# Kernel optimization log

Measured on AMD Instinct MI355X. Metric: run time of the kernel, lower is better.

The kernel has to match this reference:

```python
import jax, jax.numpy as jnp
import numpy as np

N, E, F_IN, H, G, A, OUT = 50000, 800000, 128, 256, 64, 8, 1


def _lin(k, fi, fo):
    s = 1.0 / np.sqrt(fi)
    kw, kb = jax.random.split(k)
    W = jax.random.uniform(kw, (fi, fo), jnp.float32, -s, s)
    b = jax.random.uniform(kb, (fo,), jnp.float32, -s, s)
    return W, b


def setup_inputs() -> dict:
    key = jax.random.key(0)
    ks = jax.random.split(key, 12)
    x = jax.random.normal(ks[0], (N, F_IN), jnp.float32)
    edge_index = jax.random.randint(ks[1], (2, E), 0, N, dtype=jnp.int64)
    batch = jnp.sort(jax.random.randint(ks[2], (N,), 0, G, dtype=jnp.int64))
    graph_attr = jax.random.normal(ks[3], (G, A), jnp.float32)
    W1, b1 = _lin(ks[4], F_IN, H)
    W2, b2 = _lin(ks[5], H, H)
    W3, b3 = _lin(ks[6], H, H)
    fcW1, fcb1 = _lin(ks[7], H + A, H)
    fcW2, fcb2 = _lin(ks[8], H, OUT)
    ones = jnp.ones((H,), jnp.float32)
    zeros = jnp.zeros((H,), jnp.float32)
    return dict(x=x, graph_attr=graph_attr, edge_index=edge_index, batch=batch,
                W1=W1, b1=b1, W2=W2, b2=b2, W3=W3, b3=b3,
                g1=ones, be1=zeros, g2=ones, be2=zeros, g3=ones, be3=zeros,
                fcW1=fcW1, fcb1=fcb1, fcW2=fcW2, fcb2=fcb2)


def gcn_conv(x, W, b, src, dst, n):
    # PyG GCNConv: add self-loops, symmetric normalization, xW then scatter-add
    xw = x @ W  # [N, H]
    loop = jnp.arange(n)
    src2 = jnp.concatenate([src, loop])
    dst2 = jnp.concatenate([dst, loop])
    deg = jnp.zeros((n,), xw.dtype).at[dst2].add(1.0)
    dinv = jnp.where(deg > 0, jax.lax.rsqrt(deg), 0.0)
    norm = dinv[src2] * dinv[dst2]  # [E+N]
    out = jnp.zeros((n, xw.shape[1]), xw.dtype).at[dst2].add(xw[src2] * norm[:, None])
    return out + b


def layer_norm(x, g, b, eps=1e-5):
    m = x.mean(-1, keepdims=True)
    v = ((x - m) ** 2).mean(-1, keepdims=True)
    return (x - m) * jax.lax.rsqrt(v + eps) * g + b


def reference(x, graph_attr, edge_index, batch,
              W1, b1, W2, b2, W3, b3,
              g1, be1, g2, be2, g3, be3,
              fcW1, fcb1, fcW2, fcb2):
    src, dst = edge_index[0], edge_index[1]
    h = jax.nn.relu(layer_norm(gcn_conv(x, W1, b1, src, dst, N), g1, be1))
    h = jax.nn.relu(layer_norm(gcn_conv(h, W2, b2, src, dst, N), g2, be2))
    h = jax.nn.relu(layer_norm(gcn_conv(h, W3, b3, src, dst, N), g3, be3))
    # global mean pool over graph ids
    sums = jax.ops.segment_sum(h, batch, num_segments=G)
    cnts = jax.ops.segment_sum(jnp.ones((N,), h.dtype), batch, num_segments=G)
    pooled = sums / jnp.maximum(cnts, 1.0)[:, None]  # [G, H]
    z = jnp.concatenate([pooled, graph_attr.reshape(-1, A)], axis=1)
    z = jax.nn.relu(z @ fcW1 + fcb1)
    return z @ fcW2 + fcb2  # [G, OUT]
```

## Files before the change

### kernel.cpp

```cpp
#include <hip/hip_runtime.h>
#include <hip/hip_bf16.h>

#define N_NODES 50000
#define N_EDGES 800000
#define F_IN    128
#define H_DIM   256
#define G_NUM   64
#define A_DIM   8

typedef __attribute__((ext_vector_type(8))) short short8v;
typedef __attribute__((ext_vector_type(4))) float float4v;
typedef __attribute__((ext_vector_type(2))) float float2v;

__device__ __forceinline__ float b2f(unsigned short u) {
    return __uint_as_float(((unsigned int)u) << 16);
}
__device__ __forceinline__ unsigned short f2b(float v) {
    return __hip_bfloat16_raw(__float2bfloat16(v)).x;
}
__device__ __forceinline__ unsigned char f2fp8(float v) {
    return (unsigned char)(__builtin_amdgcn_cvt_pk_fp8_f32(v, v, 0, false) & 0xff);
}
__device__ __forceinline__ unsigned int pack2(float a, float b) {
    return (unsigned int)f2b(a) | ((unsigned int)f2b(b) << 16);
}
__device__ __forceinline__ void accadd16(float2v* a, uint4 v) {
    a[0] += __builtin_amdgcn_cvt_pk_f32_fp8((int)v.x, false);
    a[1] += __builtin_amdgcn_cvt_pk_f32_fp8((int)v.x, true);
    a[2] += __builtin_amdgcn_cvt_pk_f32_fp8((int)v.y, false);
    a[3] += __builtin_amdgcn_cvt_pk_f32_fp8((int)v.y, true);
    a[4] += __builtin_amdgcn_cvt_pk_f32_fp8((int)v.z, false);
    a[5] += __builtin_amdgcn_cvt_pk_f32_fp8((int)v.z, true);
    a[6] += __builtin_amdgcn_cvt_pk_f32_fp8((int)v.w, false);
    a[7] += __builtin_amdgcn_cvt_pk_f32_fp8((int)v.w, true);
}
__device__ __forceinline__ void accadd8(float2v* a, uint2 v) {
    a[0] += __builtin_amdgcn_cvt_pk_f32_fp8((int)v.x, false);
    a[1] += __builtin_amdgcn_cvt_pk_f32_fp8((int)v.x, true);
    a[2] += __builtin_amdgcn_cvt_pk_f32_fp8((int)v.y, false);
    a[3] += __builtin_amdgcn_cvt_pk_f32_fp8((int)v.y, true);
}


__global__ void init_kernel(const int* __restrict__ dst, int* __restrict__ indeg,
                            const float* __restrict__ W1, unsigned short* __restrict__ Wt1,
                            const float* __restrict__ W2, unsigned short* __restrict__ Wt2,
                            const float* __restrict__ W3, unsigned short* __restrict__ Wt3) {
    const int EB = (N_EDGES + 255) / 256;
    const int n_w1 = F_IN * H_DIM;
    const int n_w2 = H_DIM * H_DIM;
    int b = blockIdx.x, t = threadIdx.x;
    if (b < EB) {
        int i = b * 256 + t;
        if (i < N_EDGES) atomicAdd(&indeg[dst[i]], 1);
        return;
    }
    int i = (b - EB) * 256 + t;
    if (i < n_w1) {
        int k = i / H_DIM, n = i % H_DIM;
        Wt1[(size_t)n * F_IN + k] = f2b(W1[i]);
    } else if (i < n_w1 + n_w2) {
        int j = i - n_w1;
        int k = j / H_DIM, n = j % H_DIM;
        Wt2[(size_t)n * H_DIM + k] = f2b(W2[j]);
    } else if (i < n_w1 + 2 * n_w2) {
        int j = i - n_w1 - n_w2;
        int k = j / H_DIM, n = j % H_DIM;
        Wt3[(size_t)n * H_DIM + k] = f2b(W3[j]);
    }
}


__global__ __launch_bounds__(256) void scan1_kernel(const int* __restrict__ in,
                                                    int* __restrict__ out,
                                                    int* __restrict__ bsum,
                                                    float* __restrict__ dinv, int n) {
    __shared__ int tile[256];
    int b = blockIdx.x, t = threadIdx.x, i = b * 256 + t;
    int v = (i < n) ? in[i] : 0;
    if (i < n) dinv[i] = rsqrtf((float)v + 1.0f);
    tile[t] = v;
    __syncthreads();
    #pragma unroll
    for (int o = 1; o < 256; o <<= 1) {
        int add = (t >= o) ? tile[t - o] : 0;
        __syncthreads();
        tile[t] += add;
        __syncthreads();
    }
    if (i < n) out[i] = tile[t] - v;
    if (t == 255) bsum[b] = tile[255];
}

__global__ __launch_bounds__(256) void scan2_kernel(int* __restrict__ bsum, int nb,
                                                    const int* __restrict__ batch,
                                                    int* __restrict__ gstart,
                                                    float* __restrict__ pooled) {
    __shared__ int tile[256];
    int t = threadIdx.x;
    int v = (t < nb) ? bsum[t] : 0;
    tile[t] = v;
    __syncthreads();
    #pragma unroll
    for (int o = 1; o < 256; o <<= 1) {
        int add = (t >= o) ? tile[t - o] : 0;
        __syncthreads();
        tile[t] += add;
        __syncthreads();
    }
    if (t < nb) bsum[t] = tile[t] - v;
    if (t <= G_NUM) {
        int lo = 0, hi = N_NODES;
        while (lo < hi) {
            int mid = (lo + hi) >> 1;
            if (batch[mid] < t) lo = mid + 1; else hi = mid;
        }
        gstart[t] = lo;
    }
    for (int i = t; i < G_NUM * H_DIM; i += 256) pooled[i] = 0.f;
}

__global__ __launch_bounds__(256) void scan3_kernel(int* __restrict__ out,
                                                    const int* __restrict__ bsum,
                                                    int* __restrict__ pos, int n) {
    int i = blockIdx.x * blockDim.x + threadIdx.x;
    if (i < n) {
        int r = out[i] + bsum[i >> 8];
        out[i] = r;
        pos[i] = r;
    }
    if (i == 0) out[n] = N_EDGES;
}


__global__ void place2_kernel(const int* __restrict__ src, const int* __restrict__ dst,
                              int* __restrict__ pos, unsigned short* __restrict__ csr_src,
                              const float4* __restrict__ x, unsigned int* __restrict__ xb8,
                              const float* __restrict__ dinv) {
    const int PB = (N_EDGES + 255) / 256;
    int b = blockIdx.x, t = threadIdx.x;
    if (b < PB) {
        int i = b * 256 + t;
        if (i < N_EDGES) {
            int s = src[i], dn = dst[i];
            int slot = atomicAdd(&pos[dn], 1);
            csr_src[slot] = (unsigned short)s;
        }
        return;
    }
    int i = (b - PB) * 256 + t;
    if (i < N_NODES * (F_IN / 4)) {
        float4 vv = x[i];
        float dv = dinv[i >> 5];
        unsigned int pk = (unsigned int)__builtin_amdgcn_cvt_pk_fp8_f32(vv.x * dv, vv.y * dv, 0, false);
        pk = (unsigned int)__builtin_amdgcn_cvt_pk_fp8_f32(vv.z * dv, vv.w * dv, (int)pk, true);
        xb8[i] = pk;
    }
}


#define SK 40

__global__ __launch_bounds__(512) void gemm_f8(const unsigned short* __restrict__ A,
                                               const unsigned short* __restrict__ Bt,
                                               unsigned char* __restrict__ C8,
                                               const float* __restrict__ dinv,
                                               int M, int K) {
    __shared__ unsigned short As[128][SK];
    __shared__ unsigned short Bs[256][SK];
    int t = threadIdx.x;
    int wave = t >> 6, lane = t & 63;
    int wm0 = (wave & 1) * 64, wn0 = (wave >> 1) * 64;
    int bm = blockIdx.x * 128;
    int l15 = lane & 15, lq = lane >> 4;
    float4v acc[4][4];
    #pragma unroll
    for (int i = 0; i < 4; i++)
        #pragma unroll
        for (int j = 0; j < 4; j++)
            acc[i][j] = (float4v){0.f, 0.f, 0.f, 0.f};

    for (int k0 = 0; k0 < K; k0 += 32) {
        {
            int row = t >> 2, koff = (t & 3) * 8;
            uint4 va = make_uint4(0u, 0u, 0u, 0u);
            if (bm + row < M)
                va = *(const uint4*)(A + (size_t)(bm + row) * K + k0 + koff);
            *(uint4*)&As[row][koff] = va;
        }
        #pragma unroll
        for (int h = 0; h < 2; h++) {
            int c = t + h * 512;
            int row = c >> 2, koff = (c & 3) * 8;
            uint4 vb = *(const uint4*)(Bt + (size_t)row * K + k0 + koff);
            *(uint4*)&Bs[row][koff] = vb;
        }
        __syncthreads();
        short8v af[4], bf[4];
        #pragma unroll
        for (int i = 0; i < 4; i++) {
            af[i] = *(const short8v*)&As[wm0 + i * 16 + l15][lq * 8];
            bf[i] = *(const short8v*)&Bs[wn0 + i * 16 + l15][lq * 8];
        }
        #pragma unroll
        for (int i = 0; i < 4; i++)
            #pragma unroll
            for (int j = 0; j < 4; j++)
                acc[i][j] = __builtin_amdgcn_mfma_f32_16x16x32_bf16(af[i], bf[j], acc[i][j], 0, 0, 0);
        __syncthreads();
    }
    #pragma unroll
    for (int i = 0; i < 4; i++) {
        #pragma unroll
        for (int r = 0; r < 4; r++) {
            int row = bm + wm0 + i * 16 + lq * 4 + r;
            if (row < M) {
                float dv = dinv[row];
                #pragma unroll
                for (int j = 0; j < 4; j++) {
                    int col = wn0 + j * 16 + l15;
                    C8[(size_t)row * H_DIM + col] = f2fp8(dv * acc[i][j][r]);
                }
            }
        }
    }
}


__global__ __launch_bounds__(512) void gemm_ln(const unsigned short* __restrict__ A,
                                               const unsigned short* __restrict__ Bt,
                                               unsigned short* __restrict__ C,
                                               const float* __restrict__ bias,
                                               const float* __restrict__ gamma,
                                               const float* __restrict__ beta,
                                               int M, int K) {
    __shared__ unsigned short As[128][SK];
    __shared__ unsigned short Bs[256][SK];
    __shared__ float red_s[4][128];
    __shared__ float red_ss[4][128];
    int t = threadIdx.x;
    int wave = t >> 6, lane = t & 63;
    int wm0 = (wave & 1) * 64, wn0 = (wave >> 1) * 64;
    int wn_idx = wave >> 1;
    int bm = blockIdx.x * 128;
    int l15 = lane & 15, lq = lane >> 4;
    float4v acc[4][4];
    #pragma unroll
    for (int i = 0; i < 4; i++)
        #pragma unroll
        for (int j = 0; j < 4; j++)
            acc[i][j] = (float4v){0.f, 0.f, 0.f, 0.f};

    for (int k0 = 0; k0 < K; k0 += 32) {
        {
            int row = t >> 2, koff = (t & 3) * 8;
            uint4 va = make_uint4(0u, 0u, 0u, 0u);
            if (bm + row < M)
                va = *(const uint4*)(A + (size_t)(bm + row) * K + k0 + koff);
            *(uint4*)&As[row][koff] = va;
        }
        #pragma unroll
        for (int h = 0; h < 2; h++) {
            int c = t + h * 512;
            int row = c >> 2, koff = (c & 3) * 8;
            uint4 vb = *(const uint4*)(Bt + (size_t)row * K + k0 + koff);
            *(uint4*)&Bs[row][koff] = vb;
        }
        __syncthreads();
        short8v af[4], bf[4];
        #pragma unroll
        for (int i = 0; i < 4; i++) {
            af[i] = *(const short8v*)&As[wm0 + i * 16 + l15][lq * 8];
            bf[i] = *(const short8v*)&Bs[wn0 + i * 16 + l15][lq * 8];
        }
        #pragma unroll
        for (int i = 0; i < 4; i++)
            #pragma unroll
            for (int j = 0; j < 4; j++)
                acc[i][j] = __builtin_amdgcn_mfma_f32_16x16x32_bf16(af[i], bf[j], acc[i][j], 0, 0, 0);
        __syncthreads();
    }

    float bcol[4], gcol[4], becol[4];
    #pragma unroll
    for (int j = 0; j < 4; j++) {
        int col = wn0 + j * 16 + l15;
        bcol[j] = bias[col]; gcol[j] = gamma[col]; becol[j] = beta[col];
    }
    #pragma unroll
    for (int i = 0; i < 4; i++) {
        #pragma unroll
        for (int r = 0; r < 4; r++) {
            float s = 0.f, ss = 0.f;
            #pragma unroll
            for (int j = 0; j < 4; j++) {
                float v = acc[i][j][r] + bcol[j];
                s += v; ss += v * v;
            }
            #pragma unroll
            for (int o = 1; o <= 8; o <<= 1) {
                s  += __shfl_xor(s, o, 64);
                ss += __shfl_xor(ss, o, 64);
            }
            if (l15 == 0) {
                int row = wm0 + i * 16 + lq * 4 + r;
                red_s[wn_idx][row] = s;
                red_ss[wn_idx][row] = ss;
            }
        }
    }
    __syncthreads();
    #pragma unroll
    for (int i = 0; i < 4; i++) {
        #pragma unroll
        for (int r = 0; r < 4; r++) {
            int lrow = wm0 + i * 16 + lq * 4 + r;
            int row = bm + lrow;
            if (row < M) {
                float S  = red_s[0][lrow] + red_s[1][lrow] + red_s[2][lrow] + red_s[3][lrow];
                float SS = red_ss[0][lrow] + red_ss[1][lrow] + red_ss[2][lrow] + red_ss[3][lrow];
                float mn = S * (1.f / H_DIM);
                float var = SS * (1.f / H_DIM) - mn * mn;
                float rstd = rsqrtf(var + 1e-5f);
                #pragma unroll
                for (int j = 0; j < 4; j++) {
                    int col = wn0 + j * 16 + l15;
                    float v = acc[i][j][r] + bcol[j];
                    float o = fmaxf((v - mn) * rstd * gcol[j] + becol[j], 0.f);
                    C[(size_t)row * H_DIM + col] = f2b(o);
                }
            }
        }
    }
}


template<int F, bool DO_LN>
__global__ __launch_bounds__(256) void gather_ns(const unsigned char* __restrict__ xw,
                                                 unsigned short* __restrict__ out,
                                                 const int* __restrict__ rowptr,
                                                 const unsigned short* __restrict__ csr_src,
                                                 const float* __restrict__ dinv,
                                                 const float* __restrict__ bias,
                                                 const float* __restrict__ gamma,
                                                 const float* __restrict__ beta) {
    constexpr int BPL = F / 16;
    constexpr int NF2 = BPL / 2;
    int lane = threadIdx.x & 63;
    int wave = threadIdx.x >> 6;
    int p = lane & 15;
    int gbase = lane & 48;
    int node = blockIdx.x * 16 + wave * 4 + (lane >> 4);
    int beg = rowptr[node];
    int deg = rowptr[node + 1] - beg;
    const unsigned char* xp = xw + (size_t)p * BPL;

    float2v acc2[NF2];
    #pragma unroll
    for (int k = 0; k < NF2; k++) acc2[k] = (float2v){0.f, 0.f};

    if constexpr (F == 256) {
        uint4 v = *(const uint4*)(xp + (size_t)node * F);
        accadd16(acc2, v);
    } else {
        uint2 v = *(const uint2*)(xp + (size_t)node * F);
        accadd8(acc2, v);
    }

    for (int b0 = 0; b0 < deg; b0 += 16) {
        int m = deg - b0; if (m > 16) m = 16;
        int sv = (p < m) ? (int)csr_src[beg + b0 + p] : 0;
        int j = 0;
        for (; j + 4 <= m; j += 4) {
            int s0 = __shfl(sv, gbase | j, 64);
            int s1 = __shfl(sv, gbase | (j + 1), 64);
            int s2 = __shfl(sv, gbase | (j + 2), 64);
            int s3 = __shfl(sv, gbase | (j + 3), 64);
            if constexpr (F == 256) {
                uint4 v0 = *(const uint4*)(xp + (size_t)s0 * F);
                uint4 v1 = *(const uint4*)(xp + (size_t)s1 * F);
                uint4 v2 = *(const uint4*)(xp + (size_t)s2 * F);
                uint4 v3 = *(const uint4*)(xp + (size_t)s3 * F);
                accadd16(acc2, v0); accadd16(acc2, v1);
                accadd16(acc2, v2); accadd16(acc2, v3);
            } else {
                uint2 v0 = *(const uint2*)(xp + (size_t)s0 * F);
                uint2 v1 = *(const uint2*)(xp + (size_t)s1 * F);
                uint2 v2 = *(const uint2*)(xp + (size_t)s2 * F);
                uint2 v3 = *(const uint2*)(xp + (size_t)s3 * F);
                accadd8(acc2, v0); accadd8(acc2, v1);
                accadd8(acc2, v2); accadd8(acc2, v3);
            }
        }
        for (; j < m; ++j) {
            int s0 = __shfl(sv, gbase | j, 64);
            if constexpr (F == 256) {
                uint4 v0 = *(const uint4*)(xp + (size_t)s0 * F);
                accadd16(acc2, v0);
            } else {
                uint2 v0 = *(const uint2*)(xp + (size_t)s0 * F);
                accadd8(acc2, v0);
            }
        }
    }

    float d = dinv[node];
    float v[BPL];
    #pragma unroll
    for (int k = 0; k < NF2; k++) { v[2 * k] = d * acc2[k].x; v[2 * k + 1] = d * acc2[k].y; }

    if constexpr (DO_LN) {
        #pragma unroll
        for (int q = 0; q < BPL / 4; q++) {
            float4 bi = ((const float4*)bias)[p * (BPL / 4) + q];
            v[q * 4 + 0] += bi.x; v[q * 4 + 1] += bi.y;
            v[q * 4 + 2] += bi.z; v[q * 4 + 3] += bi.w;
        }
        float s = 0.f, ss = 0.f;
        #pragma unroll
        for (int k = 0; k < BPL; k++) { s += v[k]; ss += v[k] * v[k]; }
        #pragma unroll
        for (int o = 1; o < 16; o <<= 1) {
            s  += __shfl_xor(s, o, 64);
            ss += __shfl_xor(ss, o, 64);
        }
        float mn = s * (1.f / F);
        float var = ss * (1.f / F) - mn * mn;
        float rstd = rsqrtf(var + 1e-5f);
        #pragma unroll
        for (int q = 0; q < BPL / 4; q++) {
            float4 ga = ((const float4*)gamma)[p * (BPL / 4) + q];
            float4 be = ((const float4*)beta)[p * (BPL / 4) + q];
            v[q * 4 + 0] = fmaxf((v[q * 4 + 0] - mn) * rstd * ga.x + be.x, 0.f);
            v[q * 4 + 1] = fmaxf((v[q * 4 + 1] - mn) * rstd * ga.y + be.y, 0.f);
            v[q * 4 + 2] = fmaxf((v[q * 4 + 2] - mn) * rstd * ga.z + be.z, 0.f);
            v[q * 4 + 3] = fmaxf((v[q * 4 + 3] - mn) * rstd * ga.w + be.w, 0.f);
        }
    }

    unsigned short* op = out + (size_t)node * F + p * BPL;
    uint4 o0;
    o0.x = pack2(v[0], v[1]); o0.y = pack2(v[2], v[3]);
    o0.z = pack2(v[4], v[5]); o0.w = pack2(v[6], v[7]);
    *(uint4*)op = o0;
    if constexpr (F == 256) {
        uint4 o1;
        o1.x = pack2(v[8],  v[9]);  o1.y = pack2(v[10], v[11]);
        o1.z = pack2(v[12], v[13]); o1.w = pack2(v[14], v[15]);
        *(uint4*)(op + 8) = o1;
    }
}


__global__ __launch_bounds__(128) void pool_kernel(const unsigned int* __restrict__ h32,
                                                   const int* __restrict__ batch,
                                                   float* __restrict__ pooled, int n) {
    int t = threadIdx.x;
    int start = blockIdx.x * 64;
    int end = min(start + 64, n);
    if (start >= n) return;
    int cur = batch[start];
    float a0 = 0.f, a1 = 0.f;
    for (int i = start; i < end; ++i) {
        int g = batch[i];
        if (g != cur) {
            atomicAdd(&pooled[(size_t)cur * H_DIM + 2 * t], a0);
            atomicAdd(&pooled[(size_t)cur * H_DIM + 2 * t + 1], a1);
            a0 = a1 = 0.f;
            cur = g;
        }
        unsigned int u = h32[(size_t)i * (H_DIM / 2) + t];
        a0 += b2f((unsigned short)(u & 0xffffu));
        a1 += b2f((unsigned short)(u >> 16));
    }
    atomicAdd(&pooled[(size_t)cur * H_DIM + 2 * t], a0);
    atomicAdd(&pooled[(size_t)cur * H_DIM + 2 * t + 1], a1);
}


__global__ __launch_bounds__(256) void fc_kernel(const float* __restrict__ pooled,
                                                 const int* __restrict__ gstart,
                                                 const float* __restrict__ gattr,
                                                 const float* __restrict__ fcW1,
                                                 const float* __restrict__ fcb1,
                                                 const float* __restrict__ fcW2,
                                                 const float* __restrict__ fcb2,
                                                 float* __restrict__ out) {
    __shared__ float zc[H_DIM + A_DIM];
    __shared__ float z1[H_DIM];
    int g = blockIdx.x, t = threadIdx.x;
    int c_i = gstart[g + 1] - gstart[g];
    float c = (float)(c_i > 1 ? c_i : 1);
    zc[t] = pooled[(size_t)g * H_DIM + t] / c;
    if (t < A_DIM) zc[H_DIM + t] = gattr[g * A_DIM + t];
    __syncthreads();
    float s = fcb1[t];
    for (int k = 0; k < H_DIM + A_DIM; k++)
        s += zc[k] * fcW1[(size_t)k * H_DIM + t];
    z1[t] = fmaxf(s, 0.f) * fcW2[t];
    __syncthreads();
    for (int off = 128; off; off >>= 1) {
        if (t < off) z1[t] += z1[t + off];
        __syncthreads();
    }
    if (t == 0) out[g] = z1[0] + fcb2[0];
}


extern "C" void kernel_launch(void* const* d_in, const int* in_sizes, int n_in,
                              void* d_out, int out_size, void* d_ws, size_t ws_size,
                              hipStream_t stream) {
    const float* x     = (const float*)d_in[0];
    const float* gattr = (const float*)d_in[1];
    const int*   ei    = (const int*)d_in[2];
    const int*   batch = (const int*)d_in[3];
    const float* W1 = (const float*)d_in[4];  const float* b1 = (const float*)d_in[5];
    const float* W2 = (const float*)d_in[6];  const float* b2 = (const float*)d_in[7];
    const float* W3 = (const float*)d_in[8];  const float* b3 = (const float*)d_in[9];
    const float* g1 = (const float*)d_in[10]; const float* be1 = (const float*)d_in[11];
    const float* g2 = (const float*)d_in[12]; const float* be2 = (const float*)d_in[13];
    const float* g3 = (const float*)d_in[14]; const float* be3 = (const float*)d_in[15];
    const float* fcW1 = (const float*)d_in[16]; const float* fcb1 = (const float*)d_in[17];
    const float* fcW2 = (const float*)d_in[18]; const float* fcb2 = (const float*)d_in[19];
    float* out = (float*)d_out;

    char* w = (char*)d_ws;
    unsigned char*  Pb8 = (unsigned char*)w;  w += (size_t)N_NODES * H_DIM;
    unsigned short* Hb  = (unsigned short*)w; w += (size_t)N_NODES * H_DIM * 2;
    unsigned char*  Xb8 = (unsigned char*)w;  w += (size_t)N_NODES * F_IN;
    unsigned short* AXb = (unsigned short*)w; w += (size_t)N_NODES * F_IN * 2;
    unsigned short* Wt1 = (unsigned short*)w; w += (size_t)H_DIM * F_IN * 2;
    unsigned short* Wt2 = (unsigned short*)w; w += (size_t)H_DIM * H_DIM * 2;
    unsigned short* Wt3 = (unsigned short*)w; w += (size_t)H_DIM * H_DIM * 2;
    float* dinv   = (float*)w; w += (size_t)N_NODES * 4;
    float* pooled = (float*)w; w += (size_t)G_NUM * H_DIM * 4;
    int* indeg    = (int*)w;   w += (size_t)N_NODES * 4;
    int* rowptr   = (int*)w;   w += (size_t)(N_NODES + 1) * 4;
    int* pos      = (int*)w;   w += (size_t)N_NODES * 4;
    unsigned short* csr_src = (unsigned short*)w; w += (size_t)N_EDGES * 2;
    int* gstart   = (int*)w;   w += (size_t)(G_NUM + 1) * 4;
    int* bsum     = (int*)w;   w += (size_t)256 * 4;

    const int* srcp = ei;
    const int* dstp = ei + N_EDGES;
    const int n_sblk = (N_NODES + 255) / 256;

    hipMemsetAsync(indeg, 0, (size_t)N_NODES * sizeof(int), stream);
    {
        const int EB = (N_EDGES + 255) / 256;
        int conv_tot = F_IN * H_DIM + 2 * H_DIM * H_DIM;
        int CB = (conv_tot + 255) / 256;
        init_kernel<<<EB + CB, 256, 0, stream>>>(dstp, indeg, W1, Wt1, W2, Wt2, W3, Wt3);
    }
    scan1_kernel<<<n_sblk, 256, 0, stream>>>(indeg, rowptr, bsum, dinv, N_NODES);
    scan2_kernel<<<1, 256, 0, stream>>>(bsum, n_sblk, batch, gstart, pooled);
    scan3_kernel<<<n_sblk, 256, 0, stream>>>(rowptr, bsum, pos, N_NODES);
    {
        const int PB = (N_EDGES + 255) / 256;
        const int CBX = (N_NODES * (F_IN / 4) + 255) / 256;
        place2_kernel<<<PB + CBX, 256, 0, stream>>>(srcp, dstp, pos, csr_src,
                                                    (const float4*)x, (unsigned int*)Xb8, dinv);
    }

    int gemm_blocks = (N_NODES + 127) / 128;
    int gather_blocks = N_NODES / 16;

    gather_ns<F_IN, false><<<gather_blocks, 256, 0, stream>>>(Xb8, AXb, rowptr, csr_src, dinv,
                                                              nullptr, nullptr, nullptr);
    gemm_ln<<<gemm_blocks, 512, 0, stream>>>(AXb, Wt1, Hb, b1, g1, be1, N_NODES, F_IN);

    gemm_f8<<<gemm_blocks, 512, 0, stream>>>(Hb, Wt2, Pb8, dinv, N_NODES, H_DIM);
    gather_ns<H_DIM, true><<<gather_blocks, 256, 0, stream>>>(Pb8, Hb, rowptr, csr_src, dinv,
                                                              b2, g2, be2);
    gemm_f8<<<gemm_blocks, 512, 0, stream>>>(Hb, Wt3, Pb8, dinv, N_NODES, H_DIM);
    gather_ns<H_DIM, true><<<gather_blocks, 256, 0, stream>>>(Pb8, Hb, rowptr, csr_src, dinv,
                                                              b3, g3, be3);

    pool_kernel<<<(N_NODES + 63) / 64, 128, 0, stream>>>((const unsigned int*)Hb, batch, pooled, N_NODES);
    fc_kernel<<<G_NUM, 256, 0, stream>>>(pooled, gstart, gattr, fcW1, fcb1, fcW2, fcb2, out);
}
```

Baseline: 381.3 us.

## Reorder layer 1 to GEMM-then-gather and fuse CSR placement into GEMM launch

Layer 1 now does the X·W1 GEMM first, writing dinv-scaled fp8 output, and then runs the 256-wide gather with the fused LayerNorm, the same order as layers 2 and 3. This replaces the old aggregate-then-GEMM path and removes the separate gemm_ln kernel. The in-degree atomic now records each edge's local slot, so CSR placement needs no second atomic pass. That placement runs as extra blocks inside the layer-1 GEMM launch, which removes the place2 kernel and the pos array. The cost is that the layer-1 gather moves 256 fp8 bytes per edge instead of 128, and x is now converted to bf16 in init_kernel.

```diff
diff --git a/kernel.cpp b/kernel.cpp
--- a/kernel.cpp
+++ b/kernel.cpp
@@ -34,39 +34,46 @@
     a[6] += __builtin_amdgcn_cvt_pk_f32_fp8((int)v.w, false);
     a[7] += __builtin_amdgcn_cvt_pk_f32_fp8((int)v.w, true);
 }
-__device__ __forceinline__ void accadd8(float2v* a, uint2 v) {
-    a[0] += __builtin_amdgcn_cvt_pk_f32_fp8((int)v.x, false);
-    a[1] += __builtin_amdgcn_cvt_pk_f32_fp8((int)v.x, true);
-    a[2] += __builtin_amdgcn_cvt_pk_f32_fp8((int)v.y, false);
-    a[3] += __builtin_amdgcn_cvt_pk_f32_fp8((int)v.y, true);
-}
 
 
 __global__ void init_kernel(const int* __restrict__ dst, int* __restrict__ indeg,
+                            unsigned short* __restrict__ eloc,
+                            const float4* __restrict__ x, uint2* __restrict__ xb,
                             const float* __restrict__ W1, unsigned short* __restrict__ Wt1,
                             const float* __restrict__ W2, unsigned short* __restrict__ Wt2,
                             const float* __restrict__ W3, unsigned short* __restrict__ Wt3) {
     const int EB = (N_EDGES + 255) / 256;
+    const int n_x4 = N_NODES * F_IN / 4;
     const int n_w1 = F_IN * H_DIM;
     const int n_w2 = H_DIM * H_DIM;
     int b = blockIdx.x, t = threadIdx.x;
     if (b < EB) {
         int i = b * 256 + t;
-        if (i < N_EDGES) atomicAdd(&indeg[dst[i]], 1);
+        if (i < N_EDGES)
+            eloc[i] = (unsigned short)atomicAdd(&indeg[dst[i]], 1);
         return;
     }
     int i = (b - EB) * 256 + t;
-    if (i < n_w1) {
-        int k = i / H_DIM, n = i % H_DIM;
-        Wt1[(size_t)n * F_IN + k] = f2b(W1[i]);
-    } else if (i < n_w1 + n_w2) {
-        int j = i - n_w1;
-        int k = j / H_DIM, n = j % H_DIM;
-        Wt2[(size_t)n * H_DIM + k] = f2b(W2[j]);
-    } else if (i < n_w1 + 2 * n_w2) {
-        int j = i - n_w1 - n_w2;
-        int k = j / H_DIM, n = j % H_DIM;
-        Wt3[(size_t)n * H_DIM + k] = f2b(W3[j]);
+    if (i < n_x4) {
+        float4 v = x[i];
+        uint2 o;
+        o.x = pack2(v.x, v.y);
+        o.y = pack2(v.z, v.w);
+        xb[i] = o;
+    } else {
+        int j = i - n_x4;
+        if (j < n_w1) {
+            int k = j / H_DIM, n = j % H_DIM;
+            Wt1[(size_t)n * F_IN + k] = f2b(W1[j]);
+        } else if (j < n_w1 + n_w2) {
+            int j2 = j - n_w1;
+            int k = j2 / H_DIM, n = j2 % H_DIM;
+            Wt2[(size_t)n * H_DIM + k] = f2b(W2[j2]);
+        } else if (j < n_w1 + 2 * n_w2) {
+            int j3 = j - n_w1 - n_w2;
+            int k = j3 / H_DIM, n = j3 % H_DIM;
+            Wt3[(size_t)n * H_DIM + k] = f2b(W3[j3]);
+        }
     }
 }
 
@@ -121,57 +128,25 @@
 }
 
 __global__ __launch_bounds__(256) void scan3_kernel(int* __restrict__ out,
-                                                    const int* __restrict__ bsum,
-                                                    int* __restrict__ pos, int n) {
+                                                    const int* __restrict__ bsum, int n) {
     int i = blockIdx.x * blockDim.x + threadIdx.x;
-    if (i < n) {
-        int r = out[i] + bsum[i >> 8];
-        out[i] = r;
-        pos[i] = r;
-    }
+    if (i < n) out[i] = out[i] + bsum[i >> 8];
     if (i == 0) out[n] = N_EDGES;
 }
 
 
-__global__ void place2_kernel(const int* __restrict__ src, const int* __restrict__ dst,
-                              int* __restrict__ pos, unsigned short* __restrict__ csr_src,
-                              const float4* __restrict__ x, unsigned int* __restrict__ xb8,
-                              const float* __restrict__ dinv) {
-    const int PB = (N_EDGES + 255) / 256;
-    int b = blockIdx.x, t = threadIdx.x;
-    if (b < PB) {
-        int i = b * 256 + t;
-        if (i < N_EDGES) {
-            int s = src[i], dn = dst[i];
-            int slot = atomicAdd(&pos[dn], 1);
-            csr_src[slot] = (unsigned short)s;
-        }
-        return;
-    }
-    int i = (b - PB) * 256 + t;
-    if (i < N_NODES * (F_IN / 4)) {
-        float4 vv = x[i];
-        float dv = dinv[i >> 5];
-        unsigned int pk = (unsigned int)__builtin_amdgcn_cvt_pk_fp8_f32(vv.x * dv, vv.y * dv, 0, false);
-        pk = (unsigned int)__builtin_amdgcn_cvt_pk_fp8_f32(vv.z * dv, vv.w * dv, (int)pk, true);
-        xb8[i] = pk;
-    }
-}
-
-
 #define SK 40
 
-__global__ __launch_bounds__(512) void gemm_f8(const unsigned short* __restrict__ A,
-                                               const unsigned short* __restrict__ Bt,
-                                               unsigned char* __restrict__ C8,
-                                               const float* __restrict__ dinv,
-                                               int M, int K) {
+__device__ __forceinline__ void gemm_body_f8(const unsigned short* __restrict__ A,
+                                             const unsigned short* __restrict__ Bt,
+                                             unsigned char* __restrict__ C8,
+                                             const float* __restrict__ dinv,
+                                             int M, int K, int bm) {
     __shared__ unsigned short As[128][SK];
     __shared__ unsigned short Bs[256][SK];
     int t = threadIdx.x;
     int wave = t >> 6, lane = t & 63;
     int wm0 = (wave & 1) * 64, wn0 = (wave >> 1) * 64;
-    int bm = blockIdx.x * 128;
     int l15 = lane & 15, lq = lane >> 4;
     float4v acc[4][4];
     #pragma unroll
@@ -226,111 +201,34 @@
     }
 }
 
-
-__global__ __launch_bounds__(512) void gemm_ln(const unsigned short* __restrict__ A,
+__global__ __launch_bounds__(512) void gemm_f8(const unsigned short* __restrict__ A,
                                                const unsigned short* __restrict__ Bt,
-                                               unsigned short* __restrict__ C,
-                                               const float* __restrict__ bias,
-                                               const float* __restrict__ gamma,
-                                               const float* __restrict__ beta,
+                                               unsigned char* __restrict__ C8,
+                                               const float* __restrict__ dinv,
                                                int M, int K) {
-    __shared__ unsigned short As[128][SK];
-    __shared__ unsigned short Bs[256][SK];
-    __shared__ float red_s[4][128];
-    __shared__ float red_ss[4][128];
-    int t = threadIdx.x;
-    int wave = t >> 6, lane = t & 63;
-    int wm0 = (wave & 1) * 64, wn0 = (wave >> 1) * 64;
-    int wn_idx = wave >> 1;
-    int bm = blockIdx.x * 128;
-    int l15 = lane & 15, lq = lane >> 4;
-    float4v acc[4][4];
-    #pragma unroll
-    for (int i = 0; i < 4; i++)
-        #pragma unroll
-        for (int j = 0; j < 4; j++)
-            acc[i][j] = (float4v){0.f, 0.f, 0.f, 0.f};
-
-    for (int k0 = 0; k0 < K; k0 += 32) {
-        {
-            int row = t >> 2, koff = (t & 3) * 8;
-            uint4 va = make_uint4(0u, 0u, 0u, 0u);
-            if (bm + row < M)
-                va = *(const uint4*)(A + (size_t)(bm + row) * K + k0 + koff);
-            *(uint4*)&As[row][koff] = va;
-        }
-        #pragma unroll
-        for (int h = 0; h < 2; h++) {
-            int c = t + h * 512;
-            int row = c >> 2, koff = (c & 3) * 8;
-            uint4 vb = *(const uint4*)(Bt + (size_t)row * K + k0 + koff);
-            *(uint4*)&Bs[row][koff] = vb;
-        }
-        __syncthreads();
-        short8v af[4], bf[4];
-        #pragma unroll
-        for (int i = 0; i < 4; i++) {
-            af[i] = *(const short8v*)&As[wm0 + i * 16 + l15][lq * 8];
-            bf[i] = *(const short8v*)&Bs[wn0 + i * 16 + l15][lq * 8];
-        }
-        #pragma unroll
-        for (int i = 0; i < 4; i++)
-            #pragma unroll
-            for (int j = 0; j < 4; j++)
-                acc[i][j] = __builtin_amdgcn_mfma_f32_16x16x32_bf16(af[i], bf[j], acc[i][j], 0, 0, 0);
-        __syncthreads();
-    }
-
-    float bcol[4], gcol[4], becol[4];
-    #pragma unroll
-    for (int j = 0; j < 4; j++) {
-        int col = wn0 + j * 16 + l15;
-        bcol[j] = bias[col]; gcol[j] = gamma[col]; becol[j] = beta[col];
-    }
-    #pragma unroll
-    for (int i = 0; i < 4; i++) {
-        #pragma unroll
-        for (int r = 0; r < 4; r++) {
-            float s = 0.f, ss = 0.f;
-            #pragma unroll
-            for (int j = 0; j < 4; j++) {
-                float v = acc[i][j][r] + bcol[j];
-                s += v; ss += v * v;
-            }
-            #pragma unroll
-            for (int o = 1; o <= 8; o <<= 1) {
-                s  += __shfl_xor(s, o, 64);
-                ss += __shfl_xor(ss, o, 64);
-            }
-            if (l15 == 0) {
-                int row = wm0 + i * 16 + lq * 4 + r;
-                red_s[wn_idx][row] = s;
-                red_ss[wn_idx][row] = ss;
-            }
-        }
-    }
-    __syncthreads();
-    #pragma unroll
-    for (int i = 0; i < 4; i++) {
-        #pragma unroll
-        for (int r = 0; r < 4; r++) {
-            int lrow = wm0 + i * 16 + lq * 4 + r;
-            int row = bm + lrow;
-            if (row < M) {
-                float S  = red_s[0][lrow] + red_s[1][lrow] + red_s[2][lrow] + red_s[3][lrow];
-                float SS = red_ss[0][lrow] + red_ss[1][lrow] + red_ss[2][lrow] + red_ss[3][lrow];
-                float mn = S * (1.f / H_DIM);
-                float var = SS * (1.f / H_DIM) - mn * mn;
-                float rstd = rsqrtf(var + 1e-5f);
-                #pragma unroll
-                for (int j = 0; j < 4; j++) {
-                    int col = wn0 + j * 16 + l15;
-                    float v = acc[i][j][r] + bcol[j];
-                    float o = fmaxf((v - mn) * rstd * gcol[j] + becol[j], 0.f);
-                    C[(size_t)row * H_DIM + col] = f2b(o);
-                }
-            }
-        }
+    gemm_body_f8(A, Bt, C8, dinv, M, K, blockIdx.x * 128);
+}
+
+
+__global__ __launch_bounds__(512) void fuse1_kernel(const unsigned short* __restrict__ Xb,
+                                                    const unsigned short* __restrict__ Wt1,
+                                                    unsigned char* __restrict__ P8,
+                                                    const float* __restrict__ dinv,
+                                                    const int* __restrict__ src,
+                                                    const int* __restrict__ dst,
+                                                    const unsigned short* __restrict__ eloc,
+                                                    const int* __restrict__ rowptr,
+                                                    unsigned short* __restrict__ csr_src) {
+    const int GB = (N_NODES + 127) / 128;
+    int b = blockIdx.x;
+    if (b < GB) {
+        gemm_body_f8(Xb, Wt1, P8, dinv, N_NODES, F_IN, b * 128);
+        return;
+    }
+    int i = (b - GB) * 512 + threadIdx.x;
+    if (i < N_EDGES) {
+        int d = dst[i];
+        csr_src[rowptr[d] + (int)eloc[i]] = (unsigned short)src[i];
     }
 }
 
@@ -359,12 +257,9 @@
     #pragma unroll
     for (int k = 0; k < NF2; k++) acc2[k] = (float2v){0.f, 0.f};
 
-    if constexpr (F == 256) {
+    {
         uint4 v = *(const uint4*)(xp + (size_t)node * F);
         accadd16(acc2, v);
-    } else {
-        uint2 v = *(const uint2*)(xp + (size_t)node * F);
-        accadd8(acc2, v);
     }
 
     for (int b0 = 0; b0 < deg; b0 += 16) {
@@ -376,31 +271,17 @@
             int s1 = __shfl(sv, gbase | (j + 1), 64);
             int s2 = __shfl(sv, gbase | (j + 2), 64);
             int s3 = __shfl(sv, gbase | (j + 3), 64);
-            if constexpr (F == 256) {
-                uint4 v0 = *(const uint4*)(xp + (size_t)s0 * F);
-                uint4 v1 = *(const uint4*)(xp + (size_t)s1 * F);
-                uint4 v2 = *(const uint4*)(xp + (size_t)s2 * F);
-                uint4 v3 = *(const uint4*)(xp + (size_t)s3 * F);
-                accadd16(acc2, v0); accadd16(acc2, v1);
-                accadd16(acc2, v2); accadd16(acc2, v3);
-            } else {
-                uint2 v0 = *(const uint2*)(xp + (size_t)s0 * F);
-                uint2 v1 = *(const uint2*)(xp + (size_t)s1 * F);
-                uint2 v2 = *(const uint2*)(xp + (size_t)s2 * F);
-                uint2 v3 = *(const uint2*)(xp + (size_t)s3 * F);
-                accadd8(acc2, v0); accadd8(acc2, v1);
-                accadd8(acc2, v2); accadd8(acc2, v3);
-            }
+            uint4 v0 = *(const uint4*)(xp + (size_t)s0 * F);
+            uint4 v1 = *(const uint4*)(xp + (size_t)s1 * F);
+            uint4 v2 = *(const uint4*)(xp + (size_t)s2 * F);
+            uint4 v3 = *(const uint4*)(xp + (size_t)s3 * F);
+            accadd16(acc2, v0); accadd16(acc2, v1);
+            accadd16(acc2, v2); accadd16(acc2, v3);
         }
         for (; j < m; ++j) {
             int s0 = __shfl(sv, gbase | j, 64);
-            if constexpr (F == 256) {
-                uint4 v0 = *(const uint4*)(xp + (size_t)s0 * F);
-                accadd16(acc2, v0);
-            } else {
-                uint2 v0 = *(const uint2*)(xp + (size_t)s0 * F);
-                accadd8(acc2, v0);
-            }
+            uint4 v0 = *(const uint4*)(xp + (size_t)s0 * F);
+            accadd16(acc2, v0);
         }
     }
 
@@ -527,16 +408,15 @@
     char* w = (char*)d_ws;
     unsigned char*  Pb8 = (unsigned char*)w;  w += (size_t)N_NODES * H_DIM;
     unsigned short* Hb  = (unsigned short*)w; w += (size_t)N_NODES * H_DIM * 2;
-    unsigned char*  Xb8 = (unsigned char*)w;  w += (size_t)N_NODES * F_IN;
-    unsigned short* AXb = (unsigned short*)w; w += (size_t)N_NODES * F_IN * 2;
+    unsigned short* Xb  = (unsigned short*)w; w += (size_t)N_NODES * F_IN * 2;
     unsigned short* Wt1 = (unsigned short*)w; w += (size_t)H_DIM * F_IN * 2;
     unsigned short* Wt2 = (unsigned short*)w; w += (size_t)H_DIM * H_DIM * 2;
     unsigned short* Wt3 = (unsigned short*)w; w += (size_t)H_DIM * H_DIM * 2;
     float* dinv   = (float*)w; w += (size_t)N_NODES * 4;
     float* pooled = (float*)w; w += (size_t)G_NUM * H_DIM * 4;
     int* indeg    = (int*)w;   w += (size_t)N_NODES * 4;
-    int* rowptr   = (int*)w;   w += (size_t)(N_NODES + 1) * 4;
-    int* pos      = (int*)w;   w += (size_t)N_NODES * 4;
+    int* rowptr   = (int*)w;   w += (size_t)(N_NODES + 4) * 4;
+    unsigned short* eloc    = (unsigned short*)w; w += (size_t)N_EDGES * 2;
     unsigned short* csr_src = (unsigned short*)w; w += (size_t)N_EDGES * 2;
     int* gstart   = (int*)w;   w += (size_t)(G_NUM + 1) * 4;
     int* bsum     = (int*)w;   w += (size_t)256 * 4;
@@ -548,27 +428,26 @@
     hipMemsetAsync(indeg, 0, (size_t)N_NODES * sizeof(int), stream);
     {
         const int EB = (N_EDGES + 255) / 256;
-        int conv_tot = F_IN * H_DIM + 2 * H_DIM * H_DIM;
+        int conv_tot = N_NODES * F_IN / 4 + F_IN * H_DIM + 2 * H_DIM * H_DIM;
         int CB = (conv_tot + 255) / 256;
-        init_kernel<<<EB + CB, 256, 0, stream>>>(dstp, indeg, W1, Wt1, W2, Wt2, W3, Wt3);
+        init_kernel<<<EB + CB, 256, 0, stream>>>(dstp, indeg, eloc, (const float4*)x,
+                                                 (uint2*)Xb, W1, Wt1, W2, Wt2, W3, Wt3);
     }
     scan1_kernel<<<n_sblk, 256, 0, stream>>>(indeg, rowptr, bsum, dinv, N_NODES);
     scan2_kernel<<<1, 256, 0, stream>>>(bsum, n_sblk, batch, gstart, pooled);
-    scan3_kernel<<<n_sblk, 256, 0, stream>>>(rowptr, bsum, pos, N_NODES);
-    {
-        const int PB = (N_EDGES + 255) / 256;
-        const int CBX = (N_NODES * (F_IN / 4) + 255) / 256;
-        place2_kernel<<<PB + CBX, 256, 0, stream>>>(srcp, dstp, pos, csr_src,
-                                                    (const float4*)x, (unsigned int*)Xb8, dinv);
-    }
+    scan3_kernel<<<n_sblk, 256, 0, stream>>>(rowptr, bsum, N_NODES);
 
     int gemm_blocks = (N_NODES + 127) / 128;
     int gather_blocks = N_NODES / 16;
 
-    gather_ns<F_IN, false><<<gather_blocks, 256, 0, stream>>>(Xb8, AXb, rowptr, csr_src, dinv,
-                                                              nullptr, nullptr, nullptr);
-    gemm_ln<<<gemm_blocks, 512, 0, stream>>>(AXb, Wt1, Hb, b1, g1, be1, N_NODES, F_IN);
-
+    {
+        const int PB = (N_EDGES + 511) / 512;
+        fuse1_kernel<<<gemm_blocks + PB, 512, 0, stream>>>(Xb, Wt1, Pb8, dinv,
+                                                           srcp, dstp, eloc, rowptr, csr_src);
+    }
+
+    gather_ns<H_DIM, true><<<gather_blocks, 256, 0, stream>>>(Pb8, Hb, rowptr, csr_src, dinv,
+                                                              b1, g1, be1);
     gemm_f8<<<gemm_blocks, 512, 0, stream>>>(Hb, Wt2, Pb8, dinv, N_NODES, H_DIM);
     gather_ns<H_DIM, true><<<gather_blocks, 256, 0, stream>>>(Pb8, Hb, rowptr, csr_src, dinv,
                                                               b2, g2, be2);
```

Result: faster. 367.3 us (-3.7%).
